# Kernel optimization log

Hardware: AMD Instinct MI355X
Metric: run time of the kernel (lower is better)

The kernel has to match this reference:

```python
import jax, jax.numpy as jnp
import numpy as np

HEADS = 8


def setup_inputs() -> dict:
    key = jax.random.key(0)
    ks = jax.random.split(key, 9)
    B, C, W, H = 8, 512, 32, 32
    dk = C // HEADS
    return {
        "x": jax.random.normal(ks[0], (B, C, W, H), dtype=jnp.float32),
        "wq": jax.random.normal(ks[1], (C, C), dtype=jnp.float32) * (1.0 / np.sqrt(C)),
        "bq": jax.random.normal(ks[2], (C,), dtype=jnp.float32) * 0.02,
        "wk": jax.random.normal(ks[3], (C, C), dtype=jnp.float32) * (1.0 / np.sqrt(C)),
        "bk": jax.random.normal(ks[4], (C,), dtype=jnp.float32) * 0.02,
        "wv": jax.random.normal(ks[5], (C, C), dtype=jnp.float32) * (1.0 / np.sqrt(C)),
        "bv": jax.random.normal(ks[6], (C,), dtype=jnp.float32) * 0.02,
        "rel_h": jax.random.normal(ks[7], (1, HEADS, dk, 1, H), dtype=jnp.float32),
        "rel_w": jax.random.normal(ks[8], (1, HEADS, dk, W, 1), dtype=jnp.float32),
    }


def reference(x, wq, bq, wk, bk, wv, bv, rel_h, rel_w):
    B, C, W, H = x.shape
    dk = C // HEADS
    N = W * H

    def proj(w, b):
        # 1x1 conv == per-pixel linear map over channels
        y = jnp.einsum('bchw,oc->bohw', x, w) + b[None, :, None, None]
        return y.reshape(B, HEADS, dk, N)

    q = proj(wq, bq)  # [B, h, dk, N]
    k = proj(wk, bk)
    v = proj(wv, bv)

    # content-content: q^T k -> [B, h, N, N]
    content_content = jnp.einsum('bhdn,bhdm->bhnm', q, k)

    # content-position: (rel_h + rel_w) -> [1, h, dk, W, H] -> [h, dk, N]
    pos = (rel_h + rel_w).reshape(HEADS, dk, N)
    # matmul(pos^T, q): [h, N, dk] @ [B, h, dk, N] -> [B, h, N, N]
    content_position = jnp.einsum('hdn,bhdm->bhnm', pos, q)

    energy = content_content + content_position
    attention = jax.nn.softmax(energy, axis=-1)  # softmax over last dim

    # out = v @ attention^T : [B, h, dk, N]
    out = jnp.einsum('bhdn,bhmn->bhdm', v, attention)
    return out.reshape(B, C, W, H)
```

## Files before the change

kernel.cpp:

```cpp
#include <hip/hip_runtime.h>

#define NPIX 1024
#define CC   512
#define DK   64
#define LOG2E 1.4426950408889634f

typedef __attribute__((ext_vector_type(8)))  short s16x8;
typedef __attribute__((ext_vector_type(8)))  _Float16 f16x8;
typedef __attribute__((ext_vector_type(16))) float f32x16;

union U4 { uint4 u; s16x8 v; };
union U4H { uint4 u; f16x8 v; };

__device__ __forceinline__ ushort f2bf(float f) {
  uint u = __float_as_uint(f);
  uint r = (u + 0x7fffu + ((u >> 16) & 1u)) >> 16;
  return (ushort)r;
}
__device__ __forceinline__ float bf2f(ushort h) { return __uint_as_float(((uint)h) << 16); }
__device__ __forceinline__ ushort f2h(float f) {
  union { _Float16 h; ushort u; } c;
  c.h = (_Float16)f;
  return c.u;
}
__device__ __forceinline__ float h2f(ushort u) {
  union { ushort u; _Float16 h; } c;
  c.u = u;
  return (float)c.h;
}

__device__ __forceinline__ uint cvtpk(float a, float b) {
  uint r;
  asm("v_cvt_pk_bf16_f32 %0, %1, %2" : "=v"(r) : "v"(a), "v"(b));
  return r;
}
__device__ __forceinline__ float fmax3(float a, float b, float c) {
  float d;
  asm("v_max3_f32 %0, %1, %2, %3" : "=v"(d) : "v"(a), "v"(b), "v"(c));
  return d;
}
__device__ __forceinline__ float exp2raw(float x) {
  float r;
  asm("v_exp_f32 %0, %1" : "=v"(r) : "v"(x));
  return r;
}

__device__ __forceinline__ f32x16 mfma32(s16x8 a, s16x8 b, f32x16 c) {
  return __builtin_amdgcn_mfma_f32_32x32x16_bf16(a, b, c, 0, 0, 0);
}
__device__ __forceinline__ f32x16 mfma32h(f16x8 a, f16x8 b, f32x16 c) {
  return __builtin_amdgcn_mfma_f32_32x32x16_f16(a, b, c, 0, 0, 0);
}

__device__ __forceinline__ void gl16(const void* g, void* l) {
  __builtin_amdgcn_global_load_lds(
      (const __attribute__((address_space(1))) void*)g,
      (__attribute__((address_space(3))) void*)l, 16, 0, 0);
}

__global__ void pos_kernel(const float* __restrict__ rel_h,
                           const float* __restrict__ rel_w,
                           ushort* __restrict__ posH) {
  int t = blockIdx.x * 256 + threadIdx.x;
  int g = t & 7;
  int n = (t >> 3) & (NPIX - 1);
  int h = t >> 13;
  int xw = n >> 5, yh = n & 31;
  ushort hbuf[8];
#pragma unroll
  for (int j = 0; j < 8; ++j) {
    int d = g * 8 + j;
    float v = rel_h[(h * 64 + d) * 32 + yh] + rel_w[(h * 64 + d) * 32 + xw];
    hbuf[j] = f2h(v);
  }
  size_t base = ((size_t)(h * NPIX + n)) * 64 + g * 8;
  *(uint4*)&posH[base] = *(uint4*)hbuf;
}

__global__ __launch_bounds__(256) void cvt_w_kernel(
    const float* __restrict__ wq, const float* __restrict__ wk,
    const float* __restrict__ wv,
    ushort* __restrict__ Wh, ushort* __restrict__ Wl) {
  int lin8 = blockIdx.x * 256 + threadIdx.x;
  int p = lin8 >> 15;
  int o = (lin8 & 32767) >> 6;
  int co = lin8 & 63;
  const float* Wsrc = (p == 0) ? wq : (p == 1) ? wk : wv;
  const float* src = &Wsrc[o * CC + co * 8];
  float4 f0 = *(const float4*)src;
  float4 f1 = *(const float4*)(src + 4);
  float f[8] = {f0.x, f0.y, f0.z, f0.w, f1.x, f1.y, f1.z, f1.w};
  ushort h8[8], l8[8];
#pragma unroll
  for (int j = 0; j < 8; ++j) {
    float sv = f[j] * 64.0f;
    ushort hi = f2h(sv);
    h8[j] = hi;
    l8[j] = f2h(sv - h2f(hi));
  }
  size_t dst = ((size_t)(p * CC + o)) * CC + co * 8;
  *(uint4*)&Wh[dst] = *(uint4*)h8;
  *(uint4*)&Wl[dst] = *(uint4*)l8;
}

__global__ __launch_bounds__(256) void cvt_x_kernel(
    const float* __restrict__ x, ushort* __restrict__ Xh) {
  int t = blockIdx.x * 256 + threadIdx.x;
  int nl = t & (NPIX - 1);
  int rest = t >> 10;
  int co = rest & 63;
  int b = rest >> 6;
  ushort h8[8];
#pragma unroll
  for (int j = 0; j < 8; ++j) {
    float v = x[(((size_t)(b * CC + co * 8 + j)) << 10) + nl];
    h8[j] = f2h(v);
  }
  size_t dst = (((size_t)(b * NPIX + nl)) << 9) + co * 8;
  *(uint4*)&Xh[dst] = *(uint4*)h8;
}

__global__ __launch_bounds__(256, 2) void proj_kernel(
    const ushort* __restrict__ Xh, const ushort* __restrict__ Wh,
    const ushort* __restrict__ Wl,
    const float* __restrict__ bq, const float* __restrict__ bk,
    const float* __restrict__ bv,
    ushort* __restrict__ KQh, ushort* __restrict__ Vb) {
  __shared__ __align__(16) ushort sW[128 * 128];
  __shared__ __align__(16) ushort sX[128 * 64];

  int tid = threadIdx.x;
  int lane = tid & 63;
  int w = tid >> 6;
  int col = lane & 31;
  int half = lane >> 5;
  int srow = lane >> 4;
  int sslot = lane & 15;

  int z = blockIdx.z;
  int b = z / 3, p = z % 3;
  const float* bias = (p == 0) ? bq : (p == 1) ? bk : bv;

  int n0 = blockIdx.x * 128;
  int o0 = blockIdx.y * 128;
  int wo = w >> 1;
  int wn = w & 1;

  f32x16 acc[2][2];
#pragma unroll
  for (int i = 0; i < 2; ++i)
#pragma unroll
    for (int j = 0; j < 2; ++j)
#pragma unroll
      for (int r = 0; r < 16; ++r) acc[i][j][r] = 0.f;

#pragma unroll 1
  for (int c0 = 0; c0 < CC; c0 += 64) {
#pragma unroll
    for (int i = 0; i < 8; ++i) {
      int rbase = (i * 4 + w) * 4;
      int row = rbase + srow;
      int j = sslot ^ (row & 15);
      int jc = j & 7;
      const ushort* src = (j < 8 || p == 2) ? Wh : Wl;
      size_t g = ((size_t)(p * CC + o0 + row)) * CC + c0 + jc * 8;
      gl16(src + g, (char*)sW + rbase * 256);
    }
#pragma unroll
    for (int i = 0; i < 4; ++i) {
      int rbase = i * 32 + w * 8;
      int row = rbase + (lane >> 3);
      int jc = (lane & 7) ^ (row & 7);
      size_t g = ((size_t)(b * NPIX + n0 + row)) * CC + c0 + jc * 8;
      gl16(Xh + g, (char*)sX + rbase * 128);
    }
    __syncthreads();

#pragma unroll
    for (int s = 0; s < 4; ++s) {
      if (p < 2) {
        f16x8 xa[2], wh_[2], wl_[2];
#pragma unroll
        for (int mt = 0; mt < 2; ++mt) {
          int row = wn * 64 + mt * 32 + col;
          int slot = ((s * 2 + half) ^ (row & 7)) << 4;
          xa[mt] = *(const f16x8*)((const char*)sX + row * 128 + slot);
        }
#pragma unroll
        for (int ct = 0; ct < 2; ++ct) {
          int row = wo * 64 + ct * 32 + col;
          int sh = ((s * 2 + half) ^ (row & 15)) << 4;
          int sl = ((8 + s * 2 + half) ^ (row & 15)) << 4;
          wh_[ct] = *(const f16x8*)((const char*)sW + row * 256 + sh);
          wl_[ct] = *(const f16x8*)((const char*)sW + row * 256 + sl);
        }
#pragma unroll
        for (int mt = 0; mt < 2; ++mt)
#pragma unroll
          for (int ct = 0; ct < 2; ++ct) {
            acc[mt][ct] = mfma32h(xa[mt], wh_[ct], acc[mt][ct]);
            acc[mt][ct] = mfma32h(xa[mt], wl_[ct], acc[mt][ct]);
          }
      } else {
        f16x8 wa[2], xb[2];
#pragma unroll
        for (int mt = 0; mt < 2; ++mt) {
          int row = wo * 64 + mt * 32 + col;
          int sh = ((s * 2 + half) ^ (row & 15)) << 4;
          wa[mt] = *(const f16x8*)((const char*)sW + row * 256 + sh);
        }
#pragma unroll
        for (int ct = 0; ct < 2; ++ct) {
          int row = wn * 64 + ct * 32 + col;
          int slot = ((s * 2 + half) ^ (row & 7)) << 4;
          xb[ct] = *(const f16x8*)((const char*)sX + row * 128 + slot);
        }
#pragma unroll
        for (int mt = 0; mt < 2; ++mt)
#pragma unroll
          for (int ct = 0; ct < 2; ++ct)
            acc[mt][ct] = mfma32h(wa[mt], xb[ct], acc[mt][ct]);
      }
    }
    __syncthreads();
  }

  const float INV64 = 0.015625f;
  if (p < 2) {
    float qscale = (p == 0) ? LOG2E : 1.0f;
#pragma unroll
    for (int ct = 0; ct < 2; ++ct) {
      int o = o0 + wo * 64 + ct * 32 + col;
      int bh = b * 8 + (o >> 6);
      int kk = ((p == 0) ? 64 : 0) + (o & 63);
      float bias_v = bias[o];
#pragma unroll
      for (int mt = 0; mt < 2; ++mt) {
        int nbase = n0 + wn * 64 + mt * 32;
#pragma unroll
        for (int r = 0; r < 16; ++r) {
          int n = nbase + (r & 3) + 8 * (r >> 2) + 4 * half;
          float v = (acc[mt][ct][r] * INV64 + bias_v) * qscale;
          size_t addr = (((size_t)bh << 10) + n) * 128 + kk;
          KQh[addr] = f2h(v);
        }
      }
    }
  } else {
#pragma unroll
    for (int ct = 0; ct < 2; ++ct) {
      int n = n0 + wn * 64 + ct * 32 + col;
#pragma unroll
      for (int mt = 0; mt < 2; ++mt) {
        int obase = o0 + wo * 64 + mt * 32;
#pragma unroll
        for (int r = 0; r < 16; ++r) {
          int o = obase + (r & 3) + 8 * (r >> 2) + 4 * half;
          int bh = b * 8 + (o >> 6);
          int d = o & 63;
          float v = acc[mt][ct][r] * INV64 + bias[o];
          Vb[(((size_t)(bh * 64 + d)) << 10) + n] = f2bf(v);
        }
      }
    }
  }
}

__global__ __launch_bounds__(256, 2) void attn_kernel(
    const ushort* __restrict__ KQh, const ushort* __restrict__ posH,
    const ushort* __restrict__ Vb, float* __restrict__ out) {
  __shared__ __align__(16) ushort sKh[2][64 * 128];
  __shared__ __align__(16) ushort sV[2][64 * 64];

  int tid = threadIdx.x;
  int lane = tid & 63;
  int w = tid >> 6;

  int bid = blockIdx.x;
  int wg = (bid & 7) * 64 + (bid >> 3);
  int bh = wg >> 3;
  int qb = wg & 7;
  int h = bh & 7;

  int col = lane & 31;
  int half = lane >> 5;
  int q0 = qb * 128 + w * 32;
  int q = q0 + col;

  uint4 bqh[8];
  {
    const ushort* rowQh = KQh + ((size_t)bh * NPIX + q) * 128;
#pragma unroll
    for (int s = 0; s < 4; ++s) {
      int off = 64 + s * 16 + half * 8;
      bqh[s] = *(const uint4*)(rowQh + off);
    }
    const ushort* rowPh = posH + ((size_t)(h * NPIX + q)) * 64;
#pragma unroll
    for (int s = 4; s < 8; ++s) {
      int off = (s - 4) * 16 + half * 8;
      bqh[s] = *(const uint4*)(rowPh + off);
    }
  }

  f32x16 oacc[2];
#pragma unroll
  for (int t = 0; t < 2; ++t)
#pragma unroll
    for (int r = 0; r < 16; ++r) oacc[t][r] = 0.f;
  float m_ = -1e30f, l_ = 0.f;

  int srow = lane >> 4;
  int sslot = lane & 15;

#define STAGE(bufi, k0)                                                      \
  {                                                                          \
    _Pragma("unroll")                                                        \
    for (int i = 0; i < 4; ++i) {                                            \
      int row = w * 16 + i * 4 + srow;                                       \
      size_t goff = ((size_t)bh * NPIX + (k0) + row) * 128 +                 \
                    ((sslot ^ (row & 15)) << 3);                             \
      gl16(KQh + goff, (char*)&sKh[bufi][0] + (w * 16 + i * 4) * 256);       \
    }                                                                        \
    _Pragma("unroll")                                                        \
    for (int i = 0; i < 2; ++i) {                                            \
      int d = w * 16 + i * 8 + (lane >> 3);                                  \
      int ks = (lane & 7) ^ (d & 7);                                         \
      size_t goff = ((size_t)(bh * 64 + d)) * NPIX + (k0) + (ks << 3);       \
      gl16(Vb + goff, (char*)&sV[bufi][0] + (w * 16 + i * 8) * 128);         \
    }                                                                        \
  }

  STAGE(0, 0);
  __syncthreads();

#pragma unroll 1
  for (int c = 0; c < 16; ++c) {
    int buf = c & 1;
    if (c < 15) STAGE(buf ^ 1, (c + 1) * 64);

    f32x16 sa[2];
#pragma unroll
    for (int t = 0; t < 2; ++t)
#pragma unroll
      for (int r = 0; r < 16; ++r) sa[t][r] = 0.f;

    __builtin_amdgcn_s_setprio(1);
#pragma unroll
    for (int s = 0; s < 8; ++s) {
      U4H ubh;
      ubh.u = bqh[s];
#pragma unroll
      for (int t = 0; t < 2; ++t) {
        int row = t * 32 + col;
        int slot = ((s * 2 + half) ^ (row & 15)) << 4;
        const f16x8 ah = *(const f16x8*)((const char*)&sKh[buf][0] + row * 256 + slot);
        sa[t] = mfma32h(ah, ubh.v, sa[t]);
      }
    }
    __builtin_amdgcn_s_setprio(0);

    float mxp[4];
#pragma unroll
    for (int j = 0; j < 4; ++j) {
      int ti = j >> 1;
      int b0 = (j & 1) * 8;
      float a = fmax3(sa[ti][b0 + 0], sa[ti][b0 + 1], sa[ti][b0 + 2]);
      float b1 = fmax3(sa[ti][b0 + 3], sa[ti][b0 + 4], sa[ti][b0 + 5]);
      float c1 = fmax3(sa[ti][b0 + 6], sa[ti][b0 + 7], a);
      mxp[j] = fmaxf(b1, c1);
    }
    float mx = fmaxf(fmax3(mxp[0], mxp[1], mxp[2]), mxp[3]);
    mx = fmaxf(mx, __shfl_xor(mx, 32));
    if (!__all(mx - m_ <= 11.54f)) {
      float mn = fmaxf(m_, mx);
      float sc = exp2raw(m_ - mn);
      l_ *= sc;
#pragma unroll
      for (int t = 0; t < 2; ++t)
#pragma unroll
        for (int r = 0; r < 16; ++r) oacc[t][r] *= sc;
      m_ = mn;
    }
#pragma unroll
    for (int t = 0; t < 2; ++t)
#pragma unroll
      for (int r = 0; r < 16; ++r) sa[t][r] = exp2raw(sa[t][r] - m_);
    float sp[8];
#pragma unroll
    for (int j = 0; j < 8; ++j) {
      int ti = j >> 2;
      int b0 = (j & 3) * 4;
      sp[j] = (sa[ti][b0 + 0] + sa[ti][b0 + 1]) + (sa[ti][b0 + 2] + sa[ti][b0 + 3]);
    }
    float ssum = ((sp[0] + sp[1]) + (sp[2] + sp[3])) + ((sp[4] + sp[5]) + (sp[6] + sp[7]));
    ssum += __shfl_xor(ssum, 32);
    l_ += ssum;

#pragma unroll
    for (int t = 0; t < 2; ++t) {
      uint ua[4], ub[4], xa[4], xb[4];
#pragma unroll
      for (int g = 0; g < 4; ++g) {
        ua[g] = cvtpk(sa[t][4 * g + 0], sa[t][4 * g + 1]);
        ub[g] = cvtpk(sa[t][4 * g + 2], sa[t][4 * g + 3]);
      }
#pragma unroll
      for (int g = 0; g < 4; ++g) {
        xa[g] = __shfl_xor(ua[g], 32);
        xb[g] = __shfl_xor(ub[g], 32);
      }
      __builtin_amdgcn_s_setprio(1);
#pragma unroll
      for (int st = 0; st < 2; ++st) {
        int g = st * 2 + half;
        U4 pf;
        if (half == 0) {
          pf.u.x = ua[g]; pf.u.y = ub[g]; pf.u.z = xa[g]; pf.u.w = xb[g];
        } else {
          pf.u.x = xa[g]; pf.u.y = xb[g]; pf.u.z = ua[g]; pf.u.w = ub[g];
        }
#pragma unroll
        for (int dt = 0; dt < 2; ++dt) {
          int d = dt * 32 + col;
          int slot = ((t * 4 + st * 2 + half) ^ (d & 7)) << 4;
          const s16x8 vf = *(const s16x8*)((const char*)&sV[buf][0] + d * 128 + slot);
          oacc[dt] = mfma32(vf, pf.v, oacc[dt]);
        }
      }
      __builtin_amdgcn_s_setprio(0);
    }
    __syncthreads();
  }
#undef STAGE

  float inv = 1.0f / l_;
#pragma unroll
  for (int dt = 0; dt < 2; ++dt)
#pragma unroll
    for (int r = 0; r < 16; ++r) {
      int d = dt * 32 + (r & 3) + 8 * (r >> 2) + 4 * half;
      out[((size_t)(bh * 64 + d) << 10) + q] = oacc[dt][r] * inv;
    }
}

extern "C" void kernel_launch(void* const* d_in, const int* in_sizes, int n_in,
                              void* d_out, int out_size, void* d_ws, size_t ws_size,
                              hipStream_t stream) {
  const float* x     = (const float*)d_in[0];
  const float* wq    = (const float*)d_in[1];
  const float* bq    = (const float*)d_in[2];
  const float* wk    = (const float*)d_in[3];
  const float* bk    = (const float*)d_in[4];
  const float* wv    = (const float*)d_in[5];
  const float* bv    = (const float*)d_in[6];
  const float* rel_h = (const float*)d_in[7];
  const float* rel_w = (const float*)d_in[8];
  float* out = (float*)d_out;

  const size_t MB = 1024 * 1024;
  char* ws = (char*)d_ws;
  ushort* KQh  = (ushort*)(ws);
  ushort* Vb   = (ushort*)(ws + 32 * MB);
  ushort* posH = (ushort*)(ws + 40 * MB);
  ushort* Xh   = (ushort*)(ws + 42 * MB);
  ushort* Wh   = (ushort*)(ws + 50 * MB);
  ushort* Wl   = (ushort*)(ws + 50 * MB + 1572864);

  pos_kernel<<<dim3(256), dim3(256), 0, stream>>>(rel_h, rel_w, posH);
  cvt_w_kernel<<<dim3(384), dim3(256), 0, stream>>>(wq, wk, wv, Wh, Wl);
  cvt_x_kernel<<<dim3(2048), dim3(256), 0, stream>>>(x, Xh);
  proj_kernel<<<dim3(8, 4, 24), dim3(256), 0, stream>>>(
      Xh, Wh, Wl, bq, bk, bv, KQh, Vb);
  attn_kernel<<<dim3(512), dim3(256), 0, stream>>>(KQh, posH, Vb, out);
}
```

Baseline: 98.37 us.

## Split attention over key halves with LSE combine and drop low-part weight GEMM

The attention kernel is split into two halves along the key dimension, doubling grid size to 1024 blocks. Each half writes an fp16 partial output plus a log-sum-exp value, and a new combine kernel merges them into the fp32 output. Separately, the fp16 hi/lo split of the Q/K projection weights is removed, which halves the projection MFMAs and weight loads at some cost in precision. The split adds an extra launch and partial-output traffic, and both the fp16 partial outputs and single-fp16 weights lower accuracy.

Result: slower. 100.7 us (+2.4%).

```diff
diff --git a/kernel.cpp b/kernel.cpp
--- a/kernel.cpp
+++ b/kernel.cpp
@@ -17,7 +17,6 @@
   uint r = (u + 0x7fffu + ((u >> 16) & 1u)) >> 16;
   return (ushort)r;
 }
-__device__ __forceinline__ float bf2f(ushort h) { return __uint_as_float(((uint)h) << 16); }
 __device__ __forceinline__ ushort f2h(float f) {
   union { _Float16 h; ushort u; } c;
   c.h = (_Float16)f;
@@ -79,8 +78,7 @@
 
 __global__ __launch_bounds__(256) void cvt_w_kernel(
     const float* __restrict__ wq, const float* __restrict__ wk,
-    const float* __restrict__ wv,
-    ushort* __restrict__ Wh, ushort* __restrict__ Wl) {
+    const float* __restrict__ wv, ushort* __restrict__ Wh) {
   int lin8 = blockIdx.x * 256 + threadIdx.x;
   int p = lin8 >> 15;
   int o = (lin8 & 32767) >> 6;
@@ -90,17 +88,11 @@
   float4 f0 = *(const float4*)src;
   float4 f1 = *(const float4*)(src + 4);
   float f[8] = {f0.x, f0.y, f0.z, f0.w, f1.x, f1.y, f1.z, f1.w};
-  ushort h8[8], l8[8];
-#pragma unroll
-  for (int j = 0; j < 8; ++j) {
-    float sv = f[j] * 64.0f;
-    ushort hi = f2h(sv);
-    h8[j] = hi;
-    l8[j] = f2h(sv - h2f(hi));
-  }
+  ushort h8[8];
+#pragma unroll
+  for (int j = 0; j < 8; ++j) h8[j] = f2h(f[j] * 64.0f);
   size_t dst = ((size_t)(p * CC + o)) * CC + co * 8;
   *(uint4*)&Wh[dst] = *(uint4*)h8;
-  *(uint4*)&Wl[dst] = *(uint4*)l8;
 }
 
 __global__ __launch_bounds__(256) void cvt_x_kernel(
@@ -122,7 +114,6 @@
 
 __global__ __launch_bounds__(256, 2) void proj_kernel(
     const ushort* __restrict__ Xh, const ushort* __restrict__ Wh,
-    const ushort* __restrict__ Wl,
     const float* __restrict__ bq, const float* __restrict__ bk,
     const float* __restrict__ bv,
     ushort* __restrict__ KQh, ushort* __restrict__ Vb) {
@@ -162,9 +153,8 @@
       int row = rbase + srow;
       int j = sslot ^ (row & 15);
       int jc = j & 7;
-      const ushort* src = (j < 8 || p == 2) ? Wh : Wl;
       size_t g = ((size_t)(p * CC + o0 + row)) * CC + c0 + jc * 8;
-      gl16(src + g, (char*)sW + rbase * 256);
+      gl16(Wh + g, (char*)sW + rbase * 256);
     }
 #pragma unroll
     for (int i = 0; i < 4; ++i) {
@@ -179,7 +169,7 @@
 #pragma unroll
     for (int s = 0; s < 4; ++s) {
       if (p < 2) {
-        f16x8 xa[2], wh_[2], wl_[2];
+        f16x8 xa[2], wh_[2];
 #pragma unroll
         for (int mt = 0; mt < 2; ++mt) {
           int row = wn * 64 + mt * 32 + col;
@@ -190,17 +180,13 @@
         for (int ct = 0; ct < 2; ++ct) {
           int row = wo * 64 + ct * 32 + col;
           int sh = ((s * 2 + half) ^ (row & 15)) << 4;
-          int sl = ((8 + s * 2 + half) ^ (row & 15)) << 4;
           wh_[ct] = *(const f16x8*)((const char*)sW + row * 256 + sh);
-          wl_[ct] = *(const f16x8*)((const char*)sW + row * 256 + sl);
         }
 #pragma unroll
         for (int mt = 0; mt < 2; ++mt)
 #pragma unroll
-          for (int ct = 0; ct < 2; ++ct) {
+          for (int ct = 0; ct < 2; ++ct)
             acc[mt][ct] = mfma32h(xa[mt], wh_[ct], acc[mt][ct]);
-            acc[mt][ct] = mfma32h(xa[mt], wl_[ct], acc[mt][ct]);
-          }
       } else {
         f16x8 wa[2], xb[2];
 #pragma unroll
@@ -268,7 +254,8 @@
 
 __global__ __launch_bounds__(256, 2) void attn_kernel(
     const ushort* __restrict__ KQh, const ushort* __restrict__ posH,
-    const ushort* __restrict__ Vb, float* __restrict__ out) {
+    const ushort* __restrict__ Vb,
+    ushort* __restrict__ Opart, float* __restrict__ Lw) {
   __shared__ __align__(16) ushort sKh[2][64 * 128];
   __shared__ __align__(16) ushort sV[2][64 * 64];
 
@@ -277,10 +264,12 @@
   int w = tid >> 6;
 
   int bid = blockIdx.x;
-  int wg = (bid & 7) * 64 + (bid >> 3);
-  int bh = wg >> 3;
-  int qb = wg & 7;
+  int wg = (bid & 7) * 128 + (bid >> 3);
+  int bh = wg >> 4;
+  int qb = (wg >> 1) & 7;
+  int sp = wg & 1;
   int h = bh & 7;
+  int kbase = sp * 512;
 
   int col = lane & 31;
   int half = lane >> 5;
@@ -331,13 +320,13 @@
     }                                                                        \
   }
 
-  STAGE(0, 0);
+  STAGE(0, kbase);
   __syncthreads();
 
 #pragma unroll 1
-  for (int c = 0; c < 16; ++c) {
+  for (int c = 0; c < 8; ++c) {
     int buf = c & 1;
-    if (c < 15) STAGE(buf ^ 1, (c + 1) * 64);
+    if (c < 7) STAGE(buf ^ 1, kbase + (c + 1) * 64);
 
     f32x16 sa[2];
 #pragma unroll
@@ -386,14 +375,15 @@
     for (int t = 0; t < 2; ++t)
 #pragma unroll
       for (int r = 0; r < 16; ++r) sa[t][r] = exp2raw(sa[t][r] - m_);
-    float sp[8];
+    float sp_[8];
 #pragma unroll
     for (int j = 0; j < 8; ++j) {
       int ti = j >> 2;
       int b0 = (j & 3) * 4;
-      sp[j] = (sa[ti][b0 + 0] + sa[ti][b0 + 1]) + (sa[ti][b0 + 2] + sa[ti][b0 + 3]);
-    }
-    float ssum = ((sp[0] + sp[1]) + (sp[2] + sp[3])) + ((sp[4] + sp[5]) + (sp[6] + sp[7]));
+      sp_[j] = (sa[ti][b0 + 0] + sa[ti][b0 + 1]) + (sa[ti][b0 + 2] + sa[ti][b0 + 3]);
+    }
+    float ssum = ((sp_[0] + sp_[1]) + (sp_[2] + sp_[3])) +
+                 ((sp_[4] + sp_[5]) + (sp_[6] + sp_[7]));
     ssum += __shfl_xor(ssum, 32);
     l_ += ssum;
 
@@ -435,13 +425,49 @@
 #undef STAGE
 
   float inv = 1.0f / l_;
+  size_t obase = (size_t)sp * 4194304;
 #pragma unroll
   for (int dt = 0; dt < 2; ++dt)
 #pragma unroll
     for (int r = 0; r < 16; ++r) {
       int d = dt * 32 + (r & 3) + 8 * (r >> 2) + 4 * half;
-      out[((size_t)(bh * 64 + d) << 10) + q] = oacc[dt][r] * inv;
-    }
+      Opart[obase + (((size_t)(bh * 64 + d)) << 10) + q] = f2h(oacc[dt][r] * inv);
+    }
+  if (half == 0) Lw[sp * 65536 + (bh << 10) + q] = m_ + __log2f(l_);
+}
+
+__global__ __launch_bounds__(256) void combine_kernel(
+    const ushort* __restrict__ Opart, const float* __restrict__ Lw,
+    float* __restrict__ out) {
+  int g = blockIdx.x * 256 + threadIdx.x;
+  int q8 = (g & 127) * 8;
+  int d  = (g >> 7) & 63;
+  int bh = g >> 13;
+  size_t o1 = (((size_t)(bh * 64 + d)) << 10) + q8;
+
+  uint4 a1 = *(const uint4*)&Opart[o1];
+  uint4 a2 = *(const uint4*)&Opart[4194304 + o1];
+  const ushort* p1 = (const ushort*)&a1;
+  const ushort* p2 = (const ushort*)&a2;
+
+  int lwbase = (bh << 10) + q8;
+  float4 l1a = *(const float4*)&Lw[lwbase];
+  float4 l1b = *(const float4*)&Lw[lwbase + 4];
+  float4 l2a = *(const float4*)&Lw[65536 + lwbase];
+  float4 l2b = *(const float4*)&Lw[65536 + lwbase + 4];
+  float lw1[8] = {l1a.x, l1a.y, l1a.z, l1a.w, l1b.x, l1b.y, l1b.z, l1b.w};
+  float lw2[8] = {l2a.x, l2a.y, l2a.z, l2a.w, l2b.x, l2b.y, l2b.z, l2b.w};
+
+  float o8[8];
+#pragma unroll
+  for (int j = 0; j < 8; ++j) {
+    float M = fmaxf(lw1[j], lw2[j]);
+    float w1 = exp2raw(lw1[j] - M);
+    float w2 = exp2raw(lw2[j] - M);
+    o8[j] = (w1 * h2f(p1[j]) + w2 * h2f(p2[j])) / (w1 + w2);
+  }
+  *(float4*)&out[o1]     = *(float4*)&o8[0];
+  *(float4*)&out[o1 + 4] = *(float4*)&o8[4];
 }
 
 extern "C" void kernel_launch(void* const* d_in, const int* in_sizes, int n_in,
@@ -460,17 +486,19 @@
 
   const size_t MB = 1024 * 1024;
   char* ws = (char*)d_ws;
-  ushort* KQh  = (ushort*)(ws);
-  ushort* Vb   = (ushort*)(ws + 32 * MB);
-  ushort* posH = (ushort*)(ws + 40 * MB);
-  ushort* Xh   = (ushort*)(ws + 42 * MB);
-  ushort* Wh   = (ushort*)(ws + 50 * MB);
-  ushort* Wl   = (ushort*)(ws + 50 * MB + 1572864);
+  ushort* KQh   = (ushort*)(ws);
+  ushort* Opart = (ushort*)(ws + 16 * MB);
+  ushort* Vb    = (ushort*)(ws + 32 * MB);
+  ushort* posH  = (ushort*)(ws + 40 * MB);
+  float*  Lw    = (float*)(ws + 41 * MB);
+  ushort* Xh    = (ushort*)(ws + 42 * MB);
+  ushort* Wh    = (ushort*)(ws + 50 * MB);
 
   pos_kernel<<<dim3(256), dim3(256), 0, stream>>>(rel_h, rel_w, posH);
-  cvt_w_kernel<<<dim3(384), dim3(256), 0, stream>>>(wq, wk, wv, Wh, Wl);
+  cvt_w_kernel<<<dim3(384), dim3(256), 0, stream>>>(wq, wk, wv, Wh);
   cvt_x_kernel<<<dim3(2048), dim3(256), 0, stream>>>(x, Xh);
   proj_kernel<<<dim3(8, 4, 24), dim3(256), 0, stream>>>(
-      Xh, Wh, Wl, bq, bk, bv, KQh, Vb);
-  attn_kernel<<<dim3(512), dim3(256), 0, stream>>>(KQh, posH, Vb, out);
-}
+      Xh, Wh, bq, bk, bv, KQh, Vb);
+  attn_kernel<<<dim3(1024), dim3(256), 0, stream>>>(KQh, posH, Vb, Opart, Lw);
+  combine_kernel<<<dim3(2048), dim3(256), 0, stream>>>(Opart, Lw, out);
+}
```
